# Performance work log

Measured on AMD Instinct MI355X. Metric: run time of the kernel, lower is better.

The kernel has to match this reference:

```python
import jax, jax.numpy as jnp
import numpy as np

N = 100000          # num nodes
E = 1600000         # num edges (before self loops)
IN_C = 128
OUT_C = 64
RATIO = 0.5
NEG_SLOPE = 0.2


def setup_inputs() -> dict:
    key = jax.random.key(0)
    k1, k2, k3, k4, k5 = jax.random.split(key, 5)
    x = jax.random.normal(k1, (N, IN_C), jnp.float32)
    # edges with no self loops (module removes then re-adds self loops)
    src = jax.random.randint(k2, (E,), 0, N, dtype=jnp.int32)
    off = jax.random.randint(k3, (E,), 1, N, dtype=jnp.int32)
    tgt = (src + off) % N
    edge_index = jnp.stack([src, tgt])  # [2, E], row0=source(j), row1=target(i)
    # glorot init
    s_w = float(np.sqrt(6.0 / (IN_C + OUT_C)))
    weight = jax.random.uniform(k4, (IN_C, OUT_C), jnp.float32, -s_w, s_w)
    s_a = float(np.sqrt(6.0 / (1 + 2 * OUT_C)))
    att = jax.random.uniform(k5, (1, 2 * OUT_C), jnp.float32, -s_a, s_a)
    batch = jnp.zeros((N,), jnp.int32)  # single graph
    return {"x": x, "weight": weight, "att": att,
            "edge_index": edge_index, "batch": batch, "bn": 0}


def reference(x, weight, att, edge_index, batch, bn):
    # add self loops (static shapes: E + N edges)
    loops = jnp.arange(N, dtype=edge_index.dtype)
    src = jnp.concatenate([edge_index[0], loops])  # edge_index_j (source)
    tgt = jnp.concatenate([edge_index[1], loops])  # edge_index_i (target)

    h = x @ weight                      # [N, OUT_C]
    x_j = h[src]                        # [E+N, OUT_C] gathered source feats
    x_i = h[tgt]

    # alpha = (cat([x_i, x_j]) * att).sum(-1)
    alpha = x_i @ att[0, :OUT_C] + x_j @ att[0, OUT_C:]   # [E+N]
    alpha = jnp.where(alpha > 0, alpha, NEG_SLOPE * alpha)  # leaky_relu

    # edge-softmax grouped by target node (every node has a self loop -> no empty segment)
    m = jax.ops.segment_max(alpha, tgt, num_segments=N)
    a = jnp.exp(alpha - m[tgt])
    denom = jax.ops.segment_sum(a, tgt, num_segments=N)
    alpha = a / (denom[tgt] + 1e-16)

    # node importance = sum of attention over outgoing edges (grouped by source)
    alpha_sum = jax.ops.segment_sum(alpha, src, num_segments=N)

    # topk node selection (ratio of all nodes; single graph)
    k = int(np.ceil(RATIO * N))
    _, topk_idx = jax.lax.top_k(alpha_sum, k)
    node_mask = jnp.zeros((N,), bool).at[topk_idx].set(True)

    # filter_dn: keep edges whose both endpoints survive; mask instead of compacting
    edge_mask = node_mask[src] & node_mask[tgt]
    alpha_m = jnp.where(edge_mask, alpha, 0.0)

    # weighted scatter-add aggregation to target nodes (aggr='add')
    out = jax.ops.segment_sum(alpha_m[:, None] * x_j, tgt, num_segments=N)  # [N, OUT_C]
    # bn flag is 0 -> BatchNorm skipped
    return out, edge_mask, node_mask
```

## Files before the change

kernel.cpp:

```cpp
#include <hip/hip_runtime.h>
#include <stdint.h>

#define IN_C 128
#define OUT_C 64
#define NEG_SLOPE 0.2f
#define RB 256
#define RBINS 512
#define STAGE 8192
#define NGH (RBINS * RB)
#define NGHS (RBINS * RBINS)
#define KC 16
#define GROWS 128

typedef unsigned int u32;
typedef unsigned long long u64;

__device__ __forceinline__ u32 fenc(float f) {
  u32 u = __float_as_uint(f);
  return (u & 0x80000000u) ? ~u : (u | 0x80000000u);
}
__device__ __forceinline__ u64 key64(float v, int i) {
  return (((u64)fenc(v)) << 32) | (u64)(0xffffffffu - (u32)i);
}

__global__ __launch_bounds__(128) void k_gemm(const float* __restrict__ x,
                                              const float* __restrict__ w,
                                              const float* __restrict__ att,
                                              float* __restrict__ h,
                                              float* __restrict__ ai, float* __restrict__ aj,
                                              int N) {
  __shared__ float sw[IN_C * OUT_C];
  __shared__ float sx[KC * GROWS];
  int tid = threadIdx.x;
  int rbase = blockIdx.x * GROWS;

  for (int i = tid; i < (IN_C * OUT_C) / 4; i += 128)
    ((float4*)sw)[i] = ((const float4*)w)[i];

  int cg = tid & 7, rg = tid >> 3;
  int c0 = cg * 8, r0 = rg * 8;
  float acc[8][8];
#pragma unroll
  for (int i = 0; i < 8; i++)
#pragma unroll
    for (int j = 0; j < 8; j++) acc[i][j] = 0.f;

  for (int kb = 0; kb < IN_C; kb += KC) {
    __syncthreads();
    {
      int grow = rbase + tid;
      float4 v0 = make_float4(0.f,0.f,0.f,0.f), v1 = v0, v2 = v0, v3 = v0;
      if (grow < N) {
        const float4* xp = (const float4*)&x[(size_t)grow * IN_C + kb];
        v0 = xp[0]; v1 = xp[1]; v2 = xp[2]; v3 = xp[3];
      }
      sx[ 0*GROWS + tid] = v0.x; sx[ 1*GROWS + tid] = v0.y;
      sx[ 2*GROWS + tid] = v0.z; sx[ 3*GROWS + tid] = v0.w;
      sx[ 4*GROWS + tid] = v1.x; sx[ 5*GROWS + tid] = v1.y;
      sx[ 6*GROWS + tid] = v1.z; sx[ 7*GROWS + tid] = v1.w;
      sx[ 8*GROWS + tid] = v2.x; sx[ 9*GROWS + tid] = v2.y;
      sx[10*GROWS + tid] = v2.z; sx[11*GROWS + tid] = v2.w;
      sx[12*GROWS + tid] = v3.x; sx[13*GROWS + tid] = v3.y;
      sx[14*GROWS + tid] = v3.z; sx[15*GROWS + tid] = v3.w;
    }
    __syncthreads();
#pragma unroll
    for (int kl = 0; kl < KC; ++kl) {
      int kg = kb + kl;
      float xr[8], wv[8];
      *(float4*)&xr[0] = *(const float4*)&sx[kl * GROWS + r0];
      *(float4*)&xr[4] = *(const float4*)&sx[kl * GROWS + r0 + 4];
      *(float4*)&wv[0] = *(const float4*)&sw[kg * OUT_C + c0];
      *(float4*)&wv[4] = *(const float4*)&sw[kg * OUT_C + c0 + 4];
#pragma unroll
      for (int i = 0; i < 8; ++i)
#pragma unroll
        for (int j = 0; j < 8; ++j)
          acc[i][j] += xr[i] * wv[j];
    }
  }

  float pi[8], pj[8];
#pragma unroll
  for (int i = 0; i < 8; ++i) { pi[i] = 0.f; pj[i] = 0.f; }
#pragma unroll
  for (int j = 0; j < 8; ++j) {
    float a0 = att[c0 + j], a1 = att[OUT_C + c0 + j];
#pragma unroll
    for (int i = 0; i < 8; ++i) {
      pi[i] += acc[i][j] * a0;
      pj[i] += acc[i][j] * a1;
    }
  }
#pragma unroll
  for (int o = 1; o < 8; o <<= 1) {
#pragma unroll
    for (int i = 0; i < 8; ++i) {
      pi[i] += __shfl_xor(pi[i], o);
      pj[i] += __shfl_xor(pj[i], o);
    }
  }
#pragma unroll
  for (int i = 0; i < 8; ++i) {
    int row = rbase + r0 + i;
    if (row < N) {
      *(float4*)&h[(size_t)row * OUT_C + c0]     = make_float4(acc[i][0], acc[i][1], acc[i][2], acc[i][3]);
      *(float4*)&h[(size_t)row * OUT_C + c0 + 4] = make_float4(acc[i][4], acc[i][5], acc[i][6], acc[i][7]);
      if (cg == 0) { ai[row] = pi[i]; aj[row] = pj[i]; }
    }
  }
}

__global__ __launch_bounds__(256) void k_rhist_t(const int* __restrict__ tgt,
                                                 int E, int EN, int chunk, u32* __restrict__ gh,
                                                 u32* __restrict__ hist8, u32* __restrict__ done,
                                                 u32* __restrict__ sel, u32* __restrict__ cnt, u32 k) {
  __shared__ u32 lh[RBINS];
  int tid = threadIdx.x, b = blockIdx.x;
  if (b == 0) {
    for (int i = tid; i < 2048; i += 256) hist8[i] = 0u;
    if (tid < 8) { done[tid] = 0u; cnt[tid] = 0u; }
    if (tid == 0) { sel[0] = 0u; sel[1] = 0u; sel[2] = k; sel[3] = 0u; }
  }
  for (int d = tid; d < RBINS; d += 256) lh[d] = 0u;
  __syncthreads();
  int lo = b * chunk, hi = min(lo + chunk, EN);
  for (int e = lo + tid; e < hi; e += 256) {
    int t = (e < E) ? tgt[e] : e - E;
    atomicAdd(&lh[((u32)t) >> 8], 1u);
  }
  __syncthreads();
  for (int d = tid; d < RBINS; d += 256) gh[d * RB + b] = lh[d];
}

__global__ __launch_bounds__(256) void k_scanA(const u32* __restrict__ in, u32* __restrict__ out,
                                               u32* __restrict__ bsum, int n) {
  __shared__ u32 s[256];
  int i = blockIdx.x * 256 + threadIdx.x;
  u32 v = (i < n) ? in[i] : 0u;
  s[threadIdx.x] = v;
  __syncthreads();
  for (int o = 1; o < 256; o <<= 1) {
    u32 t = (threadIdx.x >= (unsigned)o) ? s[threadIdx.x - o] : 0u;
    __syncthreads();
    s[threadIdx.x] += t;
    __syncthreads();
  }
  if (i < n) out[i] = s[threadIdx.x] - v;
  if (threadIdx.x == 255) bsum[blockIdx.x] = s[255];
}

__global__ __launch_bounds__(1024) void k_scanB(u32* __restrict__ bsum, int nb) {
  __shared__ u32 s[1024];
  int tid = threadIdx.x;
  u32 v = (tid < nb) ? bsum[tid] : 0u;
  s[tid] = v;
  __syncthreads();
  for (int o = 1; o < 1024; o <<= 1) {
    u32 t = (tid >= o) ? s[tid - o] : 0u;
    __syncthreads();
    s[tid] += t;
    __syncthreads();
  }
  if (tid < nb) bsum[tid] = s[tid] - v;
}

__global__ __launch_bounds__(256) void k_scanC(u32* __restrict__ out, const u32* __restrict__ bsum, int n) {
  int i = blockIdx.x * 256 + threadIdx.x;
  if (i < n) out[i] += bsum[blockIdx.x];
}

__global__ __launch_bounds__(256) void k_rscatter_t(const int* __restrict__ src, const int* __restrict__ tgt,
                                                    int E, int EN, int chunk,
                                                    const u32* __restrict__ gh, u32* __restrict__ bufB) {
  __shared__ u32 cnt[RBINS];
  int tid = threadIdx.x, b = blockIdx.x;
  for (int d = tid; d < RBINS; d += 256) cnt[d] = gh[d * RB + b];
  __syncthreads();
  int lo = b * chunk, hi = min(lo + chunk, EN);
  for (int e = lo + tid; e < hi; e += 256) {
    int s, t;
    if (e < E) { s = src[e]; t = tgt[e]; } else { s = t = e - E; }
    u32 p = atomicAdd(&cnt[((u32)t) >> 8], 1u);
    bufB[p] = (((u32)t & 255u) << 24) | (u32)s;
  }
}

__global__ __launch_bounds__(256) void k_rpass2(const u32* __restrict__ in, u32* __restrict__ out,
                                                const u32* __restrict__ gh, u32* __restrict__ ghs,
                                                u32* __restrict__ offT,
                                                const float* __restrict__ ai, const float* __restrict__ aj,
                                                float* __restrict__ alpha,
                                                int N, int EN) {
  __shared__ u32 hist[256];
  __shared__ u32 sc[256];
  __shared__ u32 lhs[RBINS];
  __shared__ u32 stage[STAGE];
  int tid = threadIdx.x, d = blockIdx.x;
  u32 start = gh[d * RB];
  u32 end = (d < RBINS - 1) ? gh[(d + 1) * RB] : (u32)EN;
  int sz = (int)(end - start);
  hist[tid] = 0u;
  for (int dd = tid; dd < RBINS; dd += 256) lhs[dd] = 0u;
  __syncthreads();
  for (u32 p = start + tid; p < end; p += 256) {
    u32 it = in[p];
    atomicAdd(&hist[it >> 24], 1u);
    atomicAdd(&lhs[(it & 0xffffffu) >> 8], 1u);
  }
  __syncthreads();
  for (int dd = tid; dd < RBINS; dd += 256) ghs[dd * RBINS + d] = lhs[dd];
  u32 hv = hist[tid];
  sc[tid] = hv;
  __syncthreads();
  for (int o = 1; o < 256; o <<= 1) {
    u32 t = (tid >= o) ? sc[tid - o] : 0u;
    __syncthreads();
    sc[tid] += t;
    __syncthreads();
  }
  u32 excl = sc[tid] - hv;
  int node = (d << 8) + tid;
  if (node < N) offT[node] = start + excl;
  if (node == 0) offT[N] = (u32)EN;
  hist[tid] = excl;
  __syncthreads();
  bool staged = (sz <= STAGE);
  for (u32 p = start + tid; p < end; p += 256) {
    u32 it = in[p];
    u32 lp = atomicAdd(&hist[it >> 24], 1u);
    if (staged) stage[lp] = it;
    else out[start + lp] = it;
  }
  __syncthreads();
  if (staged)
    for (int i = tid; i < sz; i += 256) out[start + i] = stage[i];
  __syncthreads();
  if (node < N) {
    int lb = (tid > 0) ? (int)sc[tid - 1] : 0;
    int le = (int)sc[tid];
    float an = ai[node];
    float mx = -1e30f;
    for (int i = lb; i < le; ++i) {
      u32 it = staged ? stage[i] : out[start + i];
      float a = an + aj[it & 0xffffffu];
      a = a > 0.f ? a : NEG_SLOPE * a;
      mx = fmaxf(mx, a);
      if (staged) stage[i] = __float_as_uint(a);
    }
    float sm = 0.f;
    for (int i = lb; i < le; ++i) {
      float a;
      if (staged) a = __uint_as_float(stage[i]);
      else {
        u32 it = out[start + i];
        a = an + aj[it & 0xffffffu];
        a = a > 0.f ? a : NEG_SLOPE * a;
      }
      float v = expf(a - mx);
      sm += v;
      if (staged) stage[i] = __float_as_uint(v);
      else alpha[start + i] = v;
    }
    float inv = 1.f / (sm + 1e-16f);
    for (int i = lb; i < le; ++i) {
      float v = staged ? __uint_as_float(stage[i]) : alpha[start + i];
      alpha[start + i] = v * inv;
    }
  }
}

__global__ __launch_bounds__(256) void k_rscatter_s(const u32* __restrict__ csr,
                                                    const float* __restrict__ alpha,
                                                    const u32* __restrict__ gh, const u32* __restrict__ ghs,
                                                    u64* __restrict__ bufB, int EN) {
  __shared__ u32 cnt[RBINS];
  int tid = threadIdx.x, d = blockIdx.x;
  for (int dd = tid; dd < RBINS; dd += 256) cnt[dd] = ghs[dd * RBINS + d];
  __syncthreads();
  u32 start = gh[d * RB];
  u32 end = (d < RBINS - 1) ? gh[(d + 1) * RB] : (u32)EN;
  for (u32 e = start + tid; e < end; e += 256) {
    u32 s = csr[e] & 0xffffffu;
    u32 p = atomicAdd(&cnt[s >> 8], 1u);
    bufB[p] = (((u64)(s & 255u)) << 32) | __float_as_uint(alpha[e]);
  }
}

__global__ __launch_bounds__(256) void k_asum_acc(const u64* __restrict__ bufB,
                                                  const u32* __restrict__ ghs,
                                                  float* __restrict__ asum, int N, int EN) {
  __shared__ float sums[256];
  int tid = threadIdx.x, d = blockIdx.x;
  u32 start = ghs[d * RBINS];
  u32 end = (d < RBINS - 1) ? ghs[(d + 1) * RBINS] : (u32)EN;
  sums[tid] = 0.f;
  __syncthreads();
  for (u32 p = start + tid; p < end; p += 256) {
    u64 it = bufB[p];
    atomicAdd(&sums[(u32)(it >> 32)], __uint_as_float((u32)it));
  }
  __syncthreads();
  int node = d * 256 + tid;
  if (node < N) asum[node] = sums[tid];
}

__global__ __launch_bounds__(256) void k_histpick(const float* __restrict__ asum,
                                                  const u32* __restrict__ list_in, const u32* __restrict__ cnt_in,
                                                  u32* __restrict__ list_out, u32* __restrict__ cnt_out,
                                                  u32* __restrict__ hist8, u32* __restrict__ done,
                                                  u32* __restrict__ sel, int N, int pass, int nblk) {
  __shared__ u32 lh[256];
  __shared__ u32 sres;
  __shared__ u32 s[256];
  int tid = threadIdx.x;
  lh[tid] = 0u;
  __syncthreads();
  u64 prefix = ((const u64*)sel)[0];
  int shift = 56 - 8 * pass;
  int n = list_in ? (int)*cnt_in : N;
  int i = blockIdx.x * 256 + tid;
  if (i < n) {
    int idx = list_in ? (int)list_in[i] : i;
    u64 k = key64(asum[idx], idx);
    bool ok = (pass == 0) || ((k >> (shift + 8)) == prefix);
    if (ok) {
      atomicAdd(&lh[(u32)(k >> shift) & 255u], 1u);
      if (list_out) {
        u32 p = atomicAdd(cnt_out, 1u);
        list_out[p] = (u32)idx;
      }
    }
  }
  __syncthreads();
  if (lh[tid]) atomicAdd(&hist8[pass * 256 + tid], lh[tid]);
  __syncthreads();
  if (tid == 0)
    sres = __hip_atomic_fetch_add(&done[pass], 1u, __ATOMIC_ACQ_REL, __HIP_MEMORY_SCOPE_AGENT);
  __syncthreads();
  if (sres == (u32)(nblk - 1)) {
    u32 krem = sel[2];
    u32 hv = __hip_atomic_load(&hist8[pass * 256 + (255 - tid)], __ATOMIC_RELAXED,
                               __HIP_MEMORY_SCOPE_AGENT);
    s[tid] = hv;
    __syncthreads();
    for (int o = 1; o < 256; o <<= 1) {
      u32 t = (tid >= o) ? s[tid - o] : 0u;
      __syncthreads();
      s[tid] += t;
      __syncthreads();
    }
    u32 cum = s[tid], prev = (tid > 0) ? s[tid - 1] : 0u;
    if (cum >= krem && prev < krem) {
      int dsel = 255 - tid;
      ((u64*)sel)[0] = (prefix << 8) | (u64)(u32)dsel;
      sel[2] = krem - prev;
    }
  }
}

__global__ __launch_bounds__(256) void k_finish(const float* __restrict__ asum,
                                                const u32* __restrict__ list, const u32* __restrict__ cntp,
                                                u32* __restrict__ sel) {
  __shared__ u64 keys[2048];
  __shared__ u32 cc;
  int tid = threadIdx.x;
  if (tid == 0) cc = 0u;
  __syncthreads();
  int n = (int)*cntp;
  u32 fsel = (u32)((const u64*)sel)[0];
  u32 krem = sel[2];
  for (int i = tid; i < n; i += 256) {
    int idx = (int)list[i];
    u64 k = key64(asum[idx], idx);
    if ((u32)(k >> 32) == fsel) {
      u32 p = atomicAdd(&cc, 1u);
      if (p < 2048) keys[p] = k;
    }
  }
  __syncthreads();
  int C = (int)min(cc, 2048u);
  for (int i = tid; i < C; i += 256) {
    u64 k = keys[i];
    u32 rank = 0;
    for (int j = 0; j < C; ++j)
      if (keys[j] > k) rank++;
    if (rank == krem - 1) ((u64*)sel)[0] = k;
  }
}

__global__ __launch_bounds__(256) void k_node_mask(const float* __restrict__ asum,
                                                   const u32* __restrict__ sel,
                                                   u32* __restrict__ nm,
                                                   float* __restrict__ out_node, int N) {
  int i = blockIdx.x * 256 + threadIdx.x;
  if (i >= N) return;
  u64 T = ((const u64*)sel)[0];
  bool m = key64(asum[i], i) >= T;
  nm[i] = m ? 1u : 0u;
  out_node[i] = m ? 1.f : 0.f;
}

__global__ __launch_bounds__(256) void k_mask(const int* __restrict__ src, const int* __restrict__ tgt,
                                              const u32* __restrict__ nm,
                                              const u32* __restrict__ csr, const float* __restrict__ alpha,
                                              float* __restrict__ out_edge, u64* __restrict__ pair,
                                              int E, int EN) {
  int e = blockIdx.x * 256 + threadIdx.x;
  if (e >= EN) return;
  int s, t;
  if (e < E) { s = src[e]; t = tgt[e]; } else { s = t = e - E; }
  out_edge[e] = (nm[s] && nm[t]) ? 1.f : 0.f;
  u32 sp = csr[e] & 0xffffffu;
  u32 ab = nm[sp] ? __float_as_uint(alpha[e]) : 0u;
  pair[e] = (((u64)sp) << 32) | ab;
}

__global__ __launch_bounds__(256) void k_aggregate(const u32* __restrict__ off,
                                                   const u64* __restrict__ pair,
                                                   const float* __restrict__ h,
                                                   const u32* __restrict__ nm,
                                                   float* __restrict__ out, int N) {
  int node = blockIdx.x * 8 + (threadIdx.x >> 5);
  int sub = threadIdx.x & 31;
  int g = sub >> 4;
  int c = sub & 15;
  if (node >= N) return;
  float4 acc = make_float4(0.f, 0.f, 0.f, 0.f);
  if (nm[node]) {
    u32 b = off[node], e2 = off[node + 1];
    for (u32 p0 = b; p0 < e2; p0 += 16) {
      u64 pr[8];
      float av[8];
      u32 sv[8];
#pragma unroll
      for (int q = 0; q < 8; ++q) {
        u32 p = p0 + q * 2 + (u32)g;
        bool ok = p < e2;
        pr[q] = pair[ok ? p : b];
        av[q] = ok ? __uint_as_float((u32)pr[q]) : 0.f;
        sv[q] = (u32)(pr[q] >> 32);
      }
      float4 hv[8];
#pragma unroll
      for (int q = 0; q < 8; ++q)
        hv[q] = *(const float4*)&h[(size_t)sv[q] * OUT_C + c * 4];
#pragma unroll
      for (int q = 0; q < 8; ++q) {
        acc.x += av[q] * hv[q].x;
        acc.y += av[q] * hv[q].y;
        acc.z += av[q] * hv[q].z;
        acc.w += av[q] * hv[q].w;
      }
    }
    acc.x += __shfl_xor(acc.x, 16);
    acc.y += __shfl_xor(acc.y, 16);
    acc.z += __shfl_xor(acc.z, 16);
    acc.w += __shfl_xor(acc.w, 16);
  }
  if (g == 0)
    *(float4*)&out[(size_t)node * OUT_C + c * 4] = acc;
}

extern "C" void kernel_launch(void* const* d_in, const int* in_sizes, int n_in,
                              void* d_out, int out_size, void* d_ws, size_t ws_size,
                              hipStream_t stream) {
  const float* x   = (const float*)d_in[0];
  const float* w   = (const float*)d_in[1];
  const float* att = (const float*)d_in[2];
  const int*   ei  = (const int*)d_in[3];

  int N = in_sizes[0] / IN_C;
  int E = in_sizes[3] / 2;
  int EN = E + N;
  const int* src = ei;
  const int* tgt = ei + E;

  float* out      = (float*)d_out;
  float* out_edge = out + (size_t)N * OUT_C;
  float* out_node = out_edge + (size_t)EN;

  char* p = (char*)d_ws;
  auto alloc = [&](size_t bytes) -> char* {
    char* r = p;
    p += (bytes + 255) & ~(size_t)255;
    return r;
  };
  float* h      = (float*)alloc((size_t)N * OUT_C * 4);
  float* ai     = (float*)alloc((size_t)N * 4);
  float* aj     = (float*)alloc((size_t)N * 4);
  u32*   bufA   = (u32*)alloc((size_t)EN * 4);
  u64*   bufB   = (u64*)alloc((size_t)EN * 8);
  float* alpha  = (float*)alloc((size_t)EN * 4);
  u32*   offT   = (u32*)alloc((size_t)(N + 1) * 4);
  u32*   gh     = (u32*)alloc((size_t)NGH * 4);
  u32*   ghs    = (u32*)alloc((size_t)NGHS * 4);
  u32*   bsum   = (u32*)alloc(2048 * 4);
  float* asum   = (float*)alloc((size_t)N * 4);
  u32*   nm     = (u32*)alloc((size_t)N * 4);
  u32*   hist8  = (u32*)alloc(2048 * 4);
  u32*   done   = (u32*)alloc(8 * 4);
  u32*   cnt    = (u32*)alloc(8 * 4);
  u32*   sel    = (u32*)alloc(256);
  u32*   listA  = (u32*)alloc((size_t)N * 4);
  u32*   listB  = (u32*)alloc((size_t)N * 4);

  u32 kSel = (u32)((N + 1) / 2);
  int chunk = (EN + RB - 1) / RB;
  int nScanT = (NGH + 255) / 256;
  int nScanS = (NGHS + 255) / 256;
  int gRow = (N + GROWS - 1) / GROWS;
  int gN = (N + 255) / 256;
  int gE = (EN + 255) / 256;
  int gNode8 = (N + 7) / 8;

  k_gemm<<<gRow, 128, 0, stream>>>(x, w, att, h, ai, aj, N);

  k_rhist_t<<<RB, 256, 0, stream>>>(tgt, E, EN, chunk, gh, hist8, done, sel, cnt, kSel);
  k_scanA<<<nScanT, 256, 0, stream>>>(gh, gh, bsum, NGH);
  k_scanB<<<1, 1024, 0, stream>>>(bsum, nScanT);
  k_scanC<<<nScanT, 256, 0, stream>>>(gh, bsum, NGH);
  k_rscatter_t<<<RB, 256, 0, stream>>>(src, tgt, E, EN, chunk, gh, (u32*)bufB);
  k_rpass2<<<RBINS, 256, 0, stream>>>((u32*)bufB, bufA, gh, ghs, offT, ai, aj, alpha, N, EN);

  k_scanA<<<nScanS, 256, 0, stream>>>(ghs, ghs, bsum, NGHS);
  k_scanB<<<1, 1024, 0, stream>>>(bsum, nScanS);
  k_scanC<<<nScanS, 256, 0, stream>>>(ghs, bsum, NGHS);
  k_rscatter_s<<<RBINS, 256, 0, stream>>>(bufA, alpha, gh, ghs, bufB, EN);
  k_asum_acc<<<RBINS, 256, 0, stream>>>(bufB, ghs, asum, N, EN);

  k_histpick<<<gN, 256, 0, stream>>>(asum, nullptr, nullptr, nullptr, nullptr,
                                     hist8, done, sel, N, 0, gN);
  k_histpick<<<gN, 256, 0, stream>>>(asum, nullptr, nullptr, listA, &cnt[1],
                                     hist8, done, sel, N, 1, gN);
  k_histpick<<<gN, 256, 0, stream>>>(asum, listA, &cnt[1], listB, &cnt[2],
                                     hist8, done, sel, N, 2, gN);
  k_histpick<<<gN, 256, 0, stream>>>(asum, listB, &cnt[2], listA, &cnt[3],
                                     hist8, done, sel, N, 3, gN);
  k_finish<<<1, 256, 0, stream>>>(asum, listA, &cnt[3], sel);

  k_node_mask<<<gN, 256, 0, stream>>>(asum, sel, nm, out_node, N);
  k_mask<<<gE, 256, 0, stream>>>(src, tgt, nm, bufA, alpha, out_edge, bufB, E, EN);
  k_aggregate<<<gNode8, 256, 0, stream>>>(offT, bufB, h, nm, out, N);
}
```

Baseline: 373.7 us.

## Fuse scan fixups, histogram pass, finish and mask kernels; simplify GEMM

Removes the scanC fixup kernels by adding block sums on the fly in consumers, folds the first top-k histogram pass into the alpha-sum kernel, merges the final selection into the last histpick pass, and replaces the node-mask/pair-building kernels by recomputing mask membership from asum and the threshold key inside the mask and aggregate kernels. The GEMM is rewritten to read x and W directly from global memory without shared-memory staging, using 256 threads with 4 rows per thread. This cuts kernel launches and intermediate buffers, at the cost of extra recomputation of key comparisons and more scattered global loads in aggregation and the GEMM.

```diff
diff --git a/kernel.cpp b/kernel.cpp
--- a/kernel.cpp
+++ b/kernel.cpp
@@ -9,8 +9,6 @@
 #define STAGE 8192
 #define NGH (RBINS * RB)
 #define NGHS (RBINS * RBINS)
-#define KC 16
-#define GROWS 128
 
 typedef unsigned int u32;
 typedef unsigned long long u64;
@@ -23,71 +21,57 @@
   return (((u64)fenc(v)) << 32) | (u64)(0xffffffffu - (u32)i);
 }
 
-__global__ __launch_bounds__(128) void k_gemm(const float* __restrict__ x,
+__global__ __launch_bounds__(256) void k_gemm(const float* __restrict__ x,
                                               const float* __restrict__ w,
                                               const float* __restrict__ att,
                                               float* __restrict__ h,
                                               float* __restrict__ ai, float* __restrict__ aj,
                                               int N) {
-  __shared__ float sw[IN_C * OUT_C];
-  __shared__ float sx[KC * GROWS];
   int tid = threadIdx.x;
-  int rbase = blockIdx.x * GROWS;
-
-  for (int i = tid; i < (IN_C * OUT_C) / 4; i += 128)
-    ((float4*)sw)[i] = ((const float4*)w)[i];
-
-  int cg = tid & 7, rg = tid >> 3;
-  int c0 = cg * 8, r0 = rg * 8;
-  float acc[8][8];
-#pragma unroll
-  for (int i = 0; i < 8; i++)
+  int cg = tid & 7, rq = tid >> 3;
+  int c0 = cg * 8;
+  int rbase = blockIdx.x * 128 + rq * 4;
+  int r[4];
+#pragma unroll
+  for (int i = 0; i < 4; ++i) r[i] = min(rbase + i, N - 1);
+
+  float acc[4][8];
+#pragma unroll
+  for (int i = 0; i < 4; i++)
 #pragma unroll
     for (int j = 0; j < 8; j++) acc[i][j] = 0.f;
 
-  for (int kb = 0; kb < IN_C; kb += KC) {
-    __syncthreads();
-    {
-      int grow = rbase + tid;
-      float4 v0 = make_float4(0.f,0.f,0.f,0.f), v1 = v0, v2 = v0, v3 = v0;
-      if (grow < N) {
-        const float4* xp = (const float4*)&x[(size_t)grow * IN_C + kb];
-        v0 = xp[0]; v1 = xp[1]; v2 = xp[2]; v3 = xp[3];
-      }
-      sx[ 0*GROWS + tid] = v0.x; sx[ 1*GROWS + tid] = v0.y;
-      sx[ 2*GROWS + tid] = v0.z; sx[ 3*GROWS + tid] = v0.w;
-      sx[ 4*GROWS + tid] = v1.x; sx[ 5*GROWS + tid] = v1.y;
-      sx[ 6*GROWS + tid] = v1.z; sx[ 7*GROWS + tid] = v1.w;
-      sx[ 8*GROWS + tid] = v2.x; sx[ 9*GROWS + tid] = v2.y;
-      sx[10*GROWS + tid] = v2.z; sx[11*GROWS + tid] = v2.w;
-      sx[12*GROWS + tid] = v3.x; sx[13*GROWS + tid] = v3.y;
-      sx[14*GROWS + tid] = v3.z; sx[15*GROWS + tid] = v3.w;
-    }
-    __syncthreads();
-#pragma unroll
-    for (int kl = 0; kl < KC; ++kl) {
-      int kg = kb + kl;
-      float xr[8], wv[8];
-      *(float4*)&xr[0] = *(const float4*)&sx[kl * GROWS + r0];
-      *(float4*)&xr[4] = *(const float4*)&sx[kl * GROWS + r0 + 4];
-      *(float4*)&wv[0] = *(const float4*)&sw[kg * OUT_C + c0];
-      *(float4*)&wv[4] = *(const float4*)&sw[kg * OUT_C + c0 + 4];
-#pragma unroll
-      for (int i = 0; i < 8; ++i)
+  for (int kb = 0; kb < IN_C; kb += 8) {
+    float xr8[4][8];
+#pragma unroll
+    for (int i = 0; i < 4; ++i) {
+      const float4* xp = (const float4*)&x[(size_t)r[i] * IN_C + kb];
+      float4 va = xp[0], vb = xp[1];
+      *(float4*)&xr8[i][0] = va;
+      *(float4*)&xr8[i][4] = vb;
+    }
+#pragma unroll
+    for (int kl = 0; kl < 8; ++kl) {
+      float wv[8];
+      const float4* wp = (const float4*)&w[(size_t)(kb + kl) * OUT_C + c0];
+      *(float4*)&wv[0] = wp[0];
+      *(float4*)&wv[4] = wp[1];
+#pragma unroll
+      for (int i = 0; i < 4; ++i)
 #pragma unroll
         for (int j = 0; j < 8; ++j)
-          acc[i][j] += xr[i] * wv[j];
-    }
-  }
-
-  float pi[8], pj[8];
-#pragma unroll
-  for (int i = 0; i < 8; ++i) { pi[i] = 0.f; pj[i] = 0.f; }
+          acc[i][j] += xr8[i][kl] * wv[j];
+    }
+  }
+
+  float pi[4], pj[4];
+#pragma unroll
+  for (int i = 0; i < 4; ++i) { pi[i] = 0.f; pj[i] = 0.f; }
 #pragma unroll
   for (int j = 0; j < 8; ++j) {
     float a0 = att[c0 + j], a1 = att[OUT_C + c0 + j];
 #pragma unroll
-    for (int i = 0; i < 8; ++i) {
+    for (int i = 0; i < 4; ++i) {
       pi[i] += acc[i][j] * a0;
       pj[i] += acc[i][j] * a1;
     }
@@ -95,14 +79,14 @@
 #pragma unroll
   for (int o = 1; o < 8; o <<= 1) {
 #pragma unroll
-    for (int i = 0; i < 8; ++i) {
+    for (int i = 0; i < 4; ++i) {
       pi[i] += __shfl_xor(pi[i], o);
       pj[i] += __shfl_xor(pj[i], o);
     }
   }
 #pragma unroll
-  for (int i = 0; i < 8; ++i) {
-    int row = rbase + r0 + i;
+  for (int i = 0; i < 4; ++i) {
+    int row = rbase + i;
     if (row < N) {
       *(float4*)&h[(size_t)row * OUT_C + c0]     = make_float4(acc[i][0], acc[i][1], acc[i][2], acc[i][3]);
       *(float4*)&h[(size_t)row * OUT_C + c0 + 4] = make_float4(acc[i][4], acc[i][5], acc[i][6], acc[i][7]);
@@ -133,11 +117,10 @@
   for (int d = tid; d < RBINS; d += 256) gh[d * RB + b] = lh[d];
 }
 
-__global__ __launch_bounds__(256) void k_scanA(const u32* __restrict__ in, u32* __restrict__ out,
-                                               u32* __restrict__ bsum, int n) {
+__global__ __launch_bounds__(256) void k_scanA(u32* __restrict__ data, u32* __restrict__ bsum, int n) {
   __shared__ u32 s[256];
   int i = blockIdx.x * 256 + threadIdx.x;
-  u32 v = (i < n) ? in[i] : 0u;
+  u32 v = (i < n) ? data[i] : 0u;
   s[threadIdx.x] = v;
   __syncthreads();
   for (int o = 1; o < 256; o <<= 1) {
@@ -146,7 +129,7 @@
     s[threadIdx.x] += t;
     __syncthreads();
   }
-  if (i < n) out[i] = s[threadIdx.x] - v;
+  if (i < n) data[i] = s[threadIdx.x] - v;
   if (threadIdx.x == 255) bsum[blockIdx.x] = s[255];
 }
 
@@ -165,17 +148,13 @@
   if (tid < nb) bsum[tid] = s[tid] - v;
 }
 
-__global__ __launch_bounds__(256) void k_scanC(u32* __restrict__ out, const u32* __restrict__ bsum, int n) {
-  int i = blockIdx.x * 256 + threadIdx.x;
-  if (i < n) out[i] += bsum[blockIdx.x];
-}
-
 __global__ __launch_bounds__(256) void k_rscatter_t(const int* __restrict__ src, const int* __restrict__ tgt,
                                                     int E, int EN, int chunk,
-                                                    const u32* __restrict__ gh, u32* __restrict__ bufB) {
+                                                    const u32* __restrict__ gh, const u32* __restrict__ bsumT,
+                                                    u32* __restrict__ bufB) {
   __shared__ u32 cnt[RBINS];
   int tid = threadIdx.x, b = blockIdx.x;
-  for (int d = tid; d < RBINS; d += 256) cnt[d] = gh[d * RB + b];
+  for (int d = tid; d < RBINS; d += 256) cnt[d] = gh[d * RB + b] + bsumT[d];
   __syncthreads();
   int lo = b * chunk, hi = min(lo + chunk, EN);
   for (int e = lo + tid; e < hi; e += 256) {
@@ -187,7 +166,8 @@
 }
 
 __global__ __launch_bounds__(256) void k_rpass2(const u32* __restrict__ in, u32* __restrict__ out,
-                                                const u32* __restrict__ gh, u32* __restrict__ ghs,
+                                                const u32* __restrict__ gh, const u32* __restrict__ bsumT,
+                                                u32* __restrict__ ghs,
                                                 u32* __restrict__ offT,
                                                 const float* __restrict__ ai, const float* __restrict__ aj,
                                                 float* __restrict__ alpha,
@@ -197,8 +177,8 @@
   __shared__ u32 lhs[RBINS];
   __shared__ u32 stage[STAGE];
   int tid = threadIdx.x, d = blockIdx.x;
-  u32 start = gh[d * RB];
-  u32 end = (d < RBINS - 1) ? gh[(d + 1) * RB] : (u32)EN;
+  u32 start = gh[d * RB] + bsumT[d];
+  u32 end = (d < RBINS - 1) ? (gh[(d + 1) * RB] + bsumT[d + 1]) : (u32)EN;
   int sz = (int)(end - start);
   hist[tid] = 0u;
   for (int dd = tid; dd < RBINS; dd += 256) lhs[dd] = 0u;
@@ -272,14 +252,16 @@
 
 __global__ __launch_bounds__(256) void k_rscatter_s(const u32* __restrict__ csr,
                                                     const float* __restrict__ alpha,
-                                                    const u32* __restrict__ gh, const u32* __restrict__ ghs,
+                                                    const u32* __restrict__ gh, const u32* __restrict__ bsumT,
+                                                    const u32* __restrict__ ghs, const u32* __restrict__ bsumS,
                                                     u64* __restrict__ bufB, int EN) {
   __shared__ u32 cnt[RBINS];
   int tid = threadIdx.x, d = blockIdx.x;
-  for (int dd = tid; dd < RBINS; dd += 256) cnt[dd] = ghs[dd * RBINS + d];
-  __syncthreads();
-  u32 start = gh[d * RB];
-  u32 end = (d < RBINS - 1) ? gh[(d + 1) * RB] : (u32)EN;
+  for (int dd = tid; dd < RBINS; dd += 256)
+    cnt[dd] = ghs[dd * RBINS + d] + bsumS[dd * 2 + (d >> 8)];
+  __syncthreads();
+  u32 start = gh[d * RB] + bsumT[d];
+  u32 end = (d < RBINS - 1) ? (gh[(d + 1) * RB] + bsumT[d + 1]) : (u32)EN;
   for (u32 e = start + tid; e < end; e += 256) {
     u32 s = csr[e] & 0xffffffu;
     u32 p = atomicAdd(&cnt[s >> 8], 1u);
@@ -288,13 +270,20 @@
 }
 
 __global__ __launch_bounds__(256) void k_asum_acc(const u64* __restrict__ bufB,
-                                                  const u32* __restrict__ ghs,
-                                                  float* __restrict__ asum, int N, int EN) {
+                                                  const u32* __restrict__ ghs, const u32* __restrict__ bsumS,
+                                                  float* __restrict__ asum,
+                                                  u32* __restrict__ hist8, u32* __restrict__ done,
+                                                  u32* __restrict__ sel,
+                                                  int N, int EN) {
   __shared__ float sums[256];
+  __shared__ u32 lh[256];
+  __shared__ u32 s[256];
+  __shared__ u32 sres;
   int tid = threadIdx.x, d = blockIdx.x;
-  u32 start = ghs[d * RBINS];
-  u32 end = (d < RBINS - 1) ? ghs[(d + 1) * RBINS] : (u32)EN;
+  u32 start = ghs[d * RBINS] + bsumS[d * 2];
+  u32 end = (d < RBINS - 1) ? (ghs[(d + 1) * RBINS] + bsumS[(d + 1) * 2]) : (u32)EN;
   sums[tid] = 0.f;
+  lh[tid] = 0u;
   __syncthreads();
   for (u32 p = start + tid; p < end; p += 256) {
     u64 it = bufB[p];
@@ -302,17 +291,48 @@
   }
   __syncthreads();
   int node = d * 256 + tid;
-  if (node < N) asum[node] = sums[tid];
+  float myv = sums[tid];
+  if (node < N) {
+    asum[node] = myv;
+    atomicAdd(&lh[fenc(myv) >> 24], 1u);
+  }
+  __syncthreads();
+  if (lh[tid]) atomicAdd(&hist8[tid], lh[tid]);
+  __syncthreads();
+  if (tid == 0)
+    sres = __hip_atomic_fetch_add(&done[0], 1u, __ATOMIC_ACQ_REL, __HIP_MEMORY_SCOPE_AGENT);
+  __syncthreads();
+  if (sres == (u32)(RBINS - 1)) {
+    u32 krem = sel[2];
+    u32 hv = __hip_atomic_load(&hist8[255 - tid], __ATOMIC_RELAXED, __HIP_MEMORY_SCOPE_AGENT);
+    s[tid] = hv;
+    __syncthreads();
+    for (int o = 1; o < 256; o <<= 1) {
+      u32 t = (tid >= o) ? s[tid - o] : 0u;
+      __syncthreads();
+      s[tid] += t;
+      __syncthreads();
+    }
+    u32 cum = s[tid], prev = (tid > 0) ? s[tid - 1] : 0u;
+    if (cum >= krem && prev < krem) {
+      ((u64*)sel)[0] = (u64)(u32)(255 - tid);
+      sel[2] = krem - prev;
+    }
+  }
 }
 
 __global__ __launch_bounds__(256) void k_histpick(const float* __restrict__ asum,
                                                   const u32* __restrict__ list_in, const u32* __restrict__ cnt_in,
                                                   u32* __restrict__ list_out, u32* __restrict__ cnt_out,
                                                   u32* __restrict__ hist8, u32* __restrict__ done,
-                                                  u32* __restrict__ sel, int N, int pass, int nblk) {
+                                                  u32* __restrict__ sel, int N, int pass, int nblk,
+                                                  int do_finish) {
   __shared__ u32 lh[256];
   __shared__ u32 sres;
   __shared__ u32 s[256];
+  __shared__ u32 sfin[2];
+  __shared__ u64 keys[2048];
+  __shared__ u32 cc;
   int tid = threadIdx.x;
   lh[tid] = 0u;
   __syncthreads();
@@ -323,8 +343,7 @@
   if (i < n) {
     int idx = list_in ? (int)list_in[i] : i;
     u64 k = key64(asum[idx], idx);
-    bool ok = (pass == 0) || ((k >> (shift + 8)) == prefix);
-    if (ok) {
+    if ((k >> (shift + 8)) == prefix) {
       atomicAdd(&lh[(u32)(k >> shift) & 255u], 1u);
       if (list_out) {
         u32 p = atomicAdd(cnt_out, 1u);
@@ -355,91 +374,81 @@
       int dsel = 255 - tid;
       ((u64*)sel)[0] = (prefix << 8) | (u64)(u32)dsel;
       sel[2] = krem - prev;
-    }
-  }
-}
-
-__global__ __launch_bounds__(256) void k_finish(const float* __restrict__ asum,
-                                                const u32* __restrict__ list, const u32* __restrict__ cntp,
-                                                u32* __restrict__ sel) {
-  __shared__ u64 keys[2048];
-  __shared__ u32 cc;
-  int tid = threadIdx.x;
-  if (tid == 0) cc = 0u;
-  __syncthreads();
-  int n = (int)*cntp;
-  u32 fsel = (u32)((const u64*)sel)[0];
-  u32 krem = sel[2];
-  for (int i = tid; i < n; i += 256) {
-    int idx = (int)list[i];
-    u64 k = key64(asum[idx], idx);
-    if ((u32)(k >> 32) == fsel) {
-      u32 p = atomicAdd(&cc, 1u);
-      if (p < 2048) keys[p] = k;
-    }
-  }
-  __syncthreads();
-  int C = (int)min(cc, 2048u);
-  for (int i = tid; i < C; i += 256) {
-    u64 k = keys[i];
-    u32 rank = 0;
-    for (int j = 0; j < C; ++j)
-      if (keys[j] > k) rank++;
-    if (rank == krem - 1) ((u64*)sel)[0] = k;
-  }
-}
-
-__global__ __launch_bounds__(256) void k_node_mask(const float* __restrict__ asum,
-                                                   const u32* __restrict__ sel,
-                                                   u32* __restrict__ nm,
-                                                   float* __restrict__ out_node, int N) {
-  int i = blockIdx.x * 256 + threadIdx.x;
-  if (i >= N) return;
-  u64 T = ((const u64*)sel)[0];
-  bool m = key64(asum[i], i) >= T;
-  nm[i] = m ? 1u : 0u;
-  out_node[i] = m ? 1.f : 0.f;
-}
-
-__global__ __launch_bounds__(256) void k_mask(const int* __restrict__ src, const int* __restrict__ tgt,
-                                              const u32* __restrict__ nm,
-                                              const u32* __restrict__ csr, const float* __restrict__ alpha,
-                                              float* __restrict__ out_edge, u64* __restrict__ pair,
-                                              int E, int EN) {
+      sfin[0] = (u32)dsel;
+      sfin[1] = krem - prev;
+    }
+    if (do_finish) {
+      __syncthreads();
+      u32 fsel = (u32)((prefix << 8) | (u64)sfin[0]);
+      u32 krem2 = sfin[1];
+      if (tid == 0) cc = 0u;
+      __syncthreads();
+      int n3 = (int)__hip_atomic_load(cnt_out, __ATOMIC_RELAXED, __HIP_MEMORY_SCOPE_AGENT);
+      for (int q = tid; q < n3; q += 256) {
+        int idx = (int)list_out[q];
+        u64 k = key64(asum[idx], idx);
+        if ((u32)(k >> 32) == fsel) {
+          u32 p = atomicAdd(&cc, 1u);
+          if (p < 2048) keys[p] = k;
+        }
+      }
+      __syncthreads();
+      int C = (int)min(cc, 2048u);
+      for (int q = tid; q < C; q += 256) {
+        u64 k = keys[q];
+        u32 rank = 0;
+        for (int j = 0; j < C; ++j)
+          if (keys[j] > k) rank++;
+        if (rank == krem2 - 1) ((u64*)sel)[0] = k;
+      }
+    }
+  }
+}
+
+__global__ __launch_bounds__(256) void k_masks(const int* __restrict__ src, const int* __restrict__ tgt,
+                                               const float* __restrict__ asum, const u32* __restrict__ sel,
+                                               float* __restrict__ out_edge, float* __restrict__ out_node,
+                                               int E, int EN, int N) {
   int e = blockIdx.x * 256 + threadIdx.x;
   if (e >= EN) return;
+  u64 T = ((const u64*)sel)[0];
   int s, t;
   if (e < E) { s = src[e]; t = tgt[e]; } else { s = t = e - E; }
-  out_edge[e] = (nm[s] && nm[t]) ? 1.f : 0.f;
-  u32 sp = csr[e] & 0xffffffu;
-  u32 ab = nm[sp] ? __float_as_uint(alpha[e]) : 0u;
-  pair[e] = (((u64)sp) << 32) | ab;
+  bool ms = key64(asum[s], s) >= T;
+  bool mt = key64(asum[t], t) >= T;
+  out_edge[e] = (ms && mt) ? 1.f : 0.f;
+  if (e < N) out_node[e] = (key64(asum[e], e) >= T) ? 1.f : 0.f;
 }
 
 __global__ __launch_bounds__(256) void k_aggregate(const u32* __restrict__ off,
-                                                   const u64* __restrict__ pair,
+                                                   const u32* __restrict__ csr,
+                                                   const float* __restrict__ alpha,
+                                                   const float* __restrict__ asum,
+                                                   const u32* __restrict__ sel,
                                                    const float* __restrict__ h,
-                                                   const u32* __restrict__ nm,
                                                    float* __restrict__ out, int N) {
   int node = blockIdx.x * 8 + (threadIdx.x >> 5);
   int sub = threadIdx.x & 31;
   int g = sub >> 4;
   int c = sub & 15;
   if (node >= N) return;
+  u64 T = ((const u64*)sel)[0];
   float4 acc = make_float4(0.f, 0.f, 0.f, 0.f);
-  if (nm[node]) {
+  if (key64(asum[node], node) >= T) {
     u32 b = off[node], e2 = off[node + 1];
     for (u32 p0 = b; p0 < e2; p0 += 16) {
-      u64 pr[8];
       float av[8];
       u32 sv[8];
 #pragma unroll
       for (int q = 0; q < 8; ++q) {
         u32 p = p0 + q * 2 + (u32)g;
         bool ok = p < e2;
-        pr[q] = pair[ok ? p : b];
-        av[q] = ok ? __uint_as_float((u32)pr[q]) : 0.f;
-        sv[q] = (u32)(pr[q] >> 32);
+        u32 pp = ok ? p : b;
+        u32 sp = csr[pp] & 0xffffffu;
+        float a = alpha[pp];
+        bool ms = key64(asum[sp], sp) >= T;
+        av[q] = (ok && ms) ? a : 0.f;
+        sv[q] = ms ? sp : 0u;
       }
       float4 hv[8];
 #pragma unroll
@@ -495,9 +504,9 @@
   u32*   offT   = (u32*)alloc((size_t)(N + 1) * 4);
   u32*   gh     = (u32*)alloc((size_t)NGH * 4);
   u32*   ghs    = (u32*)alloc((size_t)NGHS * 4);
-  u32*   bsum   = (u32*)alloc(2048 * 4);
+  u32*   bsumT  = (u32*)alloc(512 * 4);
+  u32*   bsumS  = (u32*)alloc(1024 * 4);
   float* asum   = (float*)alloc((size_t)N * 4);
-  u32*   nm     = (u32*)alloc((size_t)N * 4);
   u32*   hist8  = (u32*)alloc(2048 * 4);
   u32*   done   = (u32*)alloc(8 * 4);
   u32*   cnt    = (u32*)alloc(8 * 4);
@@ -509,37 +518,31 @@
   int chunk = (EN + RB - 1) / RB;
   int nScanT = (NGH + 255) / 256;
   int nScanS = (NGHS + 255) / 256;
-  int gRow = (N + GROWS - 1) / GROWS;
+  int gRow = (N + 127) / 128;
   int gN = (N + 255) / 256;
   int gE = (EN + 255) / 256;
   int gNode8 = (N + 7) / 8;
 
-  k_gemm<<<gRow, 128, 0, stream>>>(x, w, att, h, ai, aj, N);
+  k_gemm<<<gRow, 256, 0, stream>>>(x, w, att, h, ai, aj, N);
 
   k_rhist_t<<<RB, 256, 0, stream>>>(tgt, E, EN, chunk, gh, hist8, done, sel, cnt, kSel);
-  k_scanA<<<nScanT, 256, 0, stream>>>(gh, gh, bsum, NGH);
-  k_scanB<<<1, 1024, 0, stream>>>(bsum, nScanT);
-  k_scanC<<<nScanT, 256, 0, stream>>>(gh, bsum, NGH);
-  k_rscatter_t<<<RB, 256, 0, stream>>>(src, tgt, E, EN, chunk, gh, (u32*)bufB);
-  k_rpass2<<<RBINS, 256, 0, stream>>>((u32*)bufB, bufA, gh, ghs, offT, ai, aj, alpha, N, EN);
-
-  k_scanA<<<nScanS, 256, 0, stream>>>(ghs, ghs, bsum, NGHS);
-  k_scanB<<<1, 1024, 0, stream>>>(bsum, nScanS);
-  k_scanC<<<nScanS, 256, 0, stream>>>(ghs, bsum, NGHS);
-  k_rscatter_s<<<RBINS, 256, 0, stream>>>(bufA, alpha, gh, ghs, bufB, EN);
-  k_asum_acc<<<RBINS, 256, 0, stream>>>(bufB, ghs, asum, N, EN);
-
-  k_histpick<<<gN, 256, 0, stream>>>(asum, nullptr, nullptr, nullptr, nullptr,
-                                     hist8, done, sel, N, 0, gN);
+  k_scanA<<<nScanT, 256, 0, stream>>>(gh, bsumT, NGH);
+  k_scanB<<<1, 1024, 0, stream>>>(bsumT, nScanT);
+  k_rscatter_t<<<RB, 256, 0, stream>>>(src, tgt, E, EN, chunk, gh, bsumT, (u32*)bufB);
+  k_rpass2<<<RBINS, 256, 0, stream>>>((u32*)bufB, bufA, gh, bsumT, ghs, offT, ai, aj, alpha, N, EN);
+
+  k_scanA<<<nScanS, 256, 0, stream>>>(ghs, bsumS, NGHS);
+  k_scanB<<<1, 1024, 0, stream>>>(bsumS, nScanS);
+  k_rscatter_s<<<RBINS, 256, 0, stream>>>(bufA, alpha, gh, bsumT, ghs, bsumS, bufB, EN);
+  k_asum_acc<<<RBINS, 256, 0, stream>>>(bufB, ghs, bsumS, asum, hist8, done, sel, N, EN);
+
   k_histpick<<<gN, 256, 0, stream>>>(asum, nullptr, nullptr, listA, &cnt[1],
-                                     hist8, done, sel, N, 1, gN);
+                                     hist8, done, sel, N, 1, gN, 0);
   k_histpick<<<gN, 256, 0, stream>>>(asum, listA, &cnt[1], listB, &cnt[2],
-                                     hist8, done, sel, N, 2, gN);
+                                     hist8, done, sel, N, 2, gN, 0);
   k_histpick<<<gN, 256, 0, stream>>>(asum, listB, &cnt[2], listA, &cnt[3],
-                                     hist8, done, sel, N, 3, gN);
-  k_finish<<<1, 256, 0, stream>>>(asum, listA, &cnt[3], sel);
-
-  k_node_mask<<<gN, 256, 0, stream>>>(asum, sel, nm, out_node, N);
-  k_mask<<<gE, 256, 0, stream>>>(src, tgt, nm, bufA, alpha, out_edge, bufB, E, EN);
-  k_aggregate<<<gNode8, 256, 0, stream>>>(offT, bufB, h, nm, out, N);
-}
+                                     hist8, done, sel, N, 3, gN, 1);
+
+  k_masks<<<gE, 256, 0, stream>>>(src, tgt, asum, sel, out_edge, out_node, E, EN, N);
+  k_aggregate<<<gNode8, 256, 0, stream>>>(offT, bufA, alpha, asum, sel, h, out, N);
+}
```

Measured after the change: 379.0 us. About the same (+1.4%).
